# Optimization experiments

Measured on AMD Instinct MI355X. Metric: run time of the kernel, lower is better.

Reference implementation:

```python
import jax, jax.numpy as jnp
import numpy as np

B, N, C = 1, 256, 128        # batch, n_res, norm_channel
H, AC = 4, 32                # num_head, attention_channel


def setup_inputs() -> dict:
    key = jax.random.key(0)
    ks = jax.random.split(key, 9)
    s = 0.02
    return {
        "act": jax.random.normal(ks[0], (B, N, N, C), jnp.float32),
        "mask": jnp.ones((B, N, N), jnp.float32),
        "ln_g": jnp.ones((C,), jnp.float32),
        "ln_b": jnp.zeros((C,), jnp.float32),
        "wq": (jax.random.normal(ks[1], (C, H * AC), jnp.float32) * s),
        "wk": (jax.random.normal(ks[2], (C, H * AC), jnp.float32) * s),
        "wv": (jax.random.normal(ks[3], (C, H * AC), jnp.float32) * s),
        "w2d": (jax.random.normal(ks[4], (C, H), jnp.float32) * s),
        "wg": (jax.random.normal(ks[5], (C, H * AC), jnp.float32) * s),
        "bg": jnp.zeros((H * AC,), jnp.float32),
        "wo": (jax.random.normal(ks[6], (H * AC, C), jnp.float32) * s),
        "bo": jnp.zeros((C,), jnp.float32),
    }


def reference(act, mask, ln_g, ln_b, wq, wk, wv, w2d, wg, bg, wo, bo):
    eps = 1e-5
    mu = jnp.mean(act, axis=-1, keepdims=True)
    var = jnp.mean(jnp.square(act - mu), axis=-1, keepdims=True)
    a = (act - mu) * jax.lax.rsqrt(var + eps) * ln_g + ln_b  # LayerNorm

    b_, m_, i_, _ = a.shape
    q = (a @ wq).reshape(b_, m_, i_, H, AC)
    k = (a @ wk).reshape(b_, m_, i_, H, AC)
    v = (a @ wv).reshape(b_, m_, i_, H, AC)

    factor = 1.0 / np.sqrt(AC).astype(np.float32)
    # mask bias: [b, m, 1, 1, j]
    bias = (1e9 * (mask - 1.0))[:, :, None, None, :]
    aff = jnp.einsum('bmihc,bmjhc->bmhij', q * factor, k) + bias

    # pair bias: [b, h, i, j], broadcast over m (torch trailing-dim broadcast, b=1)
    nb = jnp.einsum('bijc,ch->bhij', a, w2d)
    weights = jax.nn.softmax(aff + nb[:, None], axis=-1)  # [b,m,h,i,j]

    g = jax.nn.sigmoid(a @ wg + bg).reshape(b_, m_, i_, H, AC)
    out = jnp.einsum('bmhqk,bmkhc->bmqhc', weights, v) * g  # [b,m,q,h,c]
    return out.reshape(b_, m_, i_, H * AC) @ wo + bo
```

## Files before the change

kernel.cpp:

```cpp
#include <hip/hip_runtime.h>
#include <hip/hip_fp16.h>
#include <math.h>


#define NRES 256
#define CCH  128
#define NROWS (NRES * NRES)
#define FACTOR 0.17677669529663687f

typedef __attribute__((ext_vector_type(8))) __bf16 bf16x8;
typedef __attribute__((ext_vector_type(4))) float f32x4;

__device__ __forceinline__ f32x4 mfma16(bf16x8 a, bf16x8 b, f32x4 c) {
    return __builtin_amdgcn_mfma_f32_16x16x32_bf16(a, b, c, 0, 0, 0);
}

union PK4 { __bf16 b[4]; uint2 u2; };
union PK2 { __bf16 b[2]; unsigned int u; };

__device__ __forceinline__ void hilo(float x, __bf16& h, __bf16& l) {
    h = (__bf16)x;
    l = (__bf16)(x - (float)h);
}

__global__ __launch_bounds__(256) void prep_kernel(
    const float* __restrict__ wq, const float* __restrict__ wk,
    const float* __restrict__ wv, const float* __restrict__ wg,
    const float* __restrict__ wo,
    __bf16* __restrict__ wph, __bf16* __restrict__ wpl)
{
    const int gid = blockIdx.x * 256 + threadIdx.x;
    const int wid = gid >> 11;
    const int rem = gid & 2047;
    const int nstrip = rem >> 8;
    const int kf = (rem >> 6) & 3;
    const int lane = rem & 63;
    const int l15 = lane & 15, quad = lane >> 4;
    const float* W = (wid == 0) ? wq : (wid == 1) ? wk :
                     (wid == 2) ? wv : (wid == 3) ? wg : wo;
    const float scale = (wid == 0) ? FACTOR : 1.0f;
    bf16x8 hb, lb;
    #pragma unroll
    for (int e = 0; e < 8; ++e) {
        int k = kf * 32 + quad * 8 + e;
        int n = nstrip * 16 + l15;
        float v = W[k * CCH + n] * scale;
        __bf16 h, l; hilo(v, h, l);
        hb[e] = h; lb[e] = l;
    }
    *(bf16x8*)&wph[(size_t)gid * 8] = hb;
    *(bf16x8*)&wpl[(size_t)gid * 8] = lb;
}

__global__ __launch_bounds__(256) void lnproj_kernel(
    const float* __restrict__ act, const float* __restrict__ ln_g,
    const float* __restrict__ ln_b, const float* __restrict__ w2d,
    const __bf16* __restrict__ wph, const float* __restrict__ bg,
    __bf16* __restrict__ qb, __bf16* __restrict__ kb,
    __bf16* __restrict__ vb, __half* __restrict__ gfh,
    float* __restrict__ nbP)
{
    __shared__ __align__(16) char smem[34816];
    const int t = threadIdx.x, w = t >> 6, lane = t & 63;
    const int l15 = lane & 15, quad = lane >> 4;
    __bf16* const aH = (__bf16*)(smem + w * 8704);
    const int r0w = blockIdx.x * 128 + w * 32;

    {
        const int row = lane >> 1, half = lane & 1;
        const int grow = r0w + row;
        const float* __restrict__ xp = act + (size_t)grow * CCH + half * 64;
        float4 x4[16];
        #pragma unroll
        for (int c = 0; c < 16; ++c) x4[c] = *(const float4*)(xp + c * 4);
        float s = 0.f, sq = 0.f;
        #pragma unroll
        for (int c = 0; c < 16; ++c) {
            s  += (x4[c].x + x4[c].y) + (x4[c].z + x4[c].w);
            sq += x4[c].x * x4[c].x + x4[c].y * x4[c].y +
                  x4[c].z * x4[c].z + x4[c].w * x4[c].w;
        }
        s  += __shfl_xor(s, 1, 64);
        sq += __shfl_xor(sq, 1, 64);
        float mu  = s * (1.0f / CCH);
        float var = fmaf(sq, 1.0f / CCH, -mu * mu);
        float rs  = rsqrtf(var + 1e-5f);
        float nb[4] = {0.f, 0.f, 0.f, 0.f};
        const float4* __restrict__ w2d4 = (const float4*)w2d;
        #pragma unroll
        for (int c2 = 0; c2 < 8; ++c2) {
            bf16x8 pk;
            #pragma unroll
            for (int cc = 0; cc < 2; ++cc) {
                const int c = c2 * 2 + cc;
                float4 g4 = *(const float4*)&ln_g[half * 64 + c * 4];
                float4 b4 = *(const float4*)&ln_b[half * 64 + c * 4];
                float* xv = (float*)&x4[c];
                float* gv = (float*)&g4;
                float* bv = (float*)&b4;
                #pragma unroll
                for (int e = 0; e < 4; ++e) {
                    float av = fmaf((xv[e] - mu) * rs, gv[e], bv[e]);
                    pk[cc * 4 + e] = (__bf16)av;
                    float4 wv = w2d4[half * 64 + c * 4 + e];
                    nb[0] = fmaf(av, wv.x, nb[0]);
                    nb[1] = fmaf(av, wv.y, nb[1]);
                    nb[2] = fmaf(av, wv.z, nb[2]);
                    nb[3] = fmaf(av, wv.w, nb[3]);
                }
            }
            *(bf16x8*)&aH[row * 136 + half * 64 + c2 * 8] = pk;
        }
        #pragma unroll
        for (int hh = 0; hh < 4; ++hh)
            nb[hh] += __shfl_xor(nb[hh], 1, 64);
        if (half == 0) {
            const int i = grow >> 8, j = grow & 255;
            #pragma unroll
            for (int hh = 0; hh < 4; ++hh) {
                size_t f = ((size_t)hh << 14) + ((size_t)(i >> 4) << 10) +
                           ((size_t)(j >> 4) << 6) + ((size_t)((j >> 2) & 3) << 4) +
                           (i & 15);
                nbP[f * 4 + (j & 3)] = nb[hh];
            }
        }
    }

    bf16x8 A0[4], A1[4];
    #pragma unroll
    for (int kf = 0; kf < 4; ++kf) {
        const int ao = l15 * 136 + kf * 32 + quad * 8;
        A0[kf] = *(const bf16x8*)&aH[ao];
        A1[kf] = *(const bf16x8*)&aH[ao + 16 * 136];
    }

    #pragma unroll 1
    for (int tn = 0; tn < 4; ++tn) {
        const __bf16* __restrict__ Bh = wph + (size_t)tn * 16384;
        f32x4 acc0[8], acc1[8];
        #pragma unroll
        for (int n = 0; n < 8; ++n) {
            acc0[n] = (f32x4){0.f, 0.f, 0.f, 0.f};
            acc1[n] = (f32x4){0.f, 0.f, 0.f, 0.f};
        }
        #pragma unroll
        for (int kf = 0; kf < 4; ++kf)
            #pragma unroll
            for (int n = 0; n < 8; ++n) {
                bf16x8 bh = *(const bf16x8*)&Bh[(size_t)((n * 4 + kf) * 64 + lane) * 8];
                acc0[n] = mfma16(A0[kf], bh, acc0[n]);
                acc1[n] = mfma16(A1[kf], bh, acc1[n]);
            }

        if (tn == 3) {
            __half* const sth = (__half*)aH;
            #pragma unroll 1
            for (int sp = 0; sp < 2; ++sp) {
                f32x4* accp = sp ? acc1 : acc0;
                #pragma unroll
                for (int n = 0; n < 8; ++n)
                    #pragma unroll
                    for (int r = 0; r < 4; ++r) {
                        float v = accp[n][r] + bg[n * 16 + l15];
                        sth[(quad * 4 + r) * 136 + n * 16 + l15] =
                            (__half)(1.0f / (1.0f + __expf(-v)));
                    }
                #pragma unroll
                for (int i = 0; i < 4; ++i) {
                    int row = i * 4 + (lane >> 4);
                    int c8 = lane & 15;
                    uint4 hv = *(const uint4*)&sth[row * 136 + c8 * 8];
                    *(uint4*)&gfh[(size_t)(r0w + sp * 16 + row) * CCH + c8 * 8] = hv;
                }
            }
        } else {
            __bf16* const sth = (__bf16*)aH;
            __bf16* const oh = (tn == 0) ? qb : (tn == 1) ? kb : vb;
            #pragma unroll 1
            for (int sp = 0; sp < 2; ++sp) {
                f32x4* accp = sp ? acc1 : acc0;
                #pragma unroll
                for (int n = 0; n < 8; ++n)
                    #pragma unroll
                    for (int r = 0; r < 4; ++r)
                        sth[(quad * 4 + r) * 136 + n * 16 + l15] = (__bf16)accp[n][r];
                #pragma unroll
                for (int i = 0; i < 4; ++i) {
                    int row = i * 4 + (lane >> 4);
                    int c8 = lane & 15;
                    uint4 hv = *(const uint4*)&sth[row * 136 + c8 * 8];
                    *(uint4*)&oh[(size_t)(r0w + sp * 16 + row) * CCH + c8 * 8] = hv;
                }
            }
        }
    }
}

__global__ __launch_bounds__(256) void attn_kernel(
    const __bf16* __restrict__ qb, const __bf16* __restrict__ kb,
    const __bf16* __restrict__ vb, const __half* __restrict__ gfh,
    const float* __restrict__ mask, const float* __restrict__ nbP,
    __bf16* __restrict__ gth, __bf16* __restrict__ gtl)
{
    __shared__ __align__(16) char smem[23040];
    __bf16* const vth = (__bf16*)smem;
    __bf16* const pbb = (__bf16*)(smem + 16896);
    float*  const biasrow = (float*)(smem + 22016);
    const int t = threadIdx.x, w = t >> 6, lane = t & 63;
    const int l15 = lane & 15, quad = lane >> 4;
    const int mrow = blockIdx.x >> 2, h = blockIdx.x & 3;
    const size_t rbase = (size_t)mrow * NRES;
    const int ch0 = h * 32;

    biasrow[t] = 1e9f * (mask[mrow * NRES + t] - 1.0f);

    #pragma unroll
    for (int it = 0; it < 4; ++it) {
        int f = t + it * 256;
        int j = f >> 2, cg = f & 3;
        bf16x8 hv = *(const bf16x8*)&vb[(rbase + j) * CCH + ch0 + cg * 8];
        #pragma unroll
        for (int e = 0; e < 8; ++e)
            vth[(cg * 8 + e) * 264 + j] = hv[e];
    }
    __syncthreads();

    const int i0 = w * 64;
    bf16x8 Qh[4];
    #pragma unroll
    for (int s = 0; s < 4; ++s)
        Qh[s] = *(const bf16x8*)&qb[(rbase + i0 + s * 16 + l15) * CCH + ch0 + quad * 8];

    f32x4 O[4][2];
    float ls[4] = {0.f, 0.f, 0.f, 0.f};
    #pragma unroll
    for (int s = 0; s < 4; ++s) {
        O[s][0] = (f32x4){0.f, 0.f, 0.f, 0.f};
        O[s][1] = (f32x4){0.f, 0.f, 0.f, 0.f};
    }
    __bf16* const ph = pbb + w * 640;

    for (int jb = 0; jb < NRES; jb += 32) {
        bf16x8 Kh[2];
        #pragma unroll
        for (int js = 0; js < 2; ++js)
            Kh[js] = *(const bf16x8*)&kb[(rbase + jb + js * 16 + l15) * CCH + ch0 + quad * 8];
        bf16x8 Vh2[2];
        #pragma unroll
        for (int c = 0; c < 2; ++c)
            Vh2[c] = *(const bf16x8*)&vth[(c * 16 + l15) * 264 + jb + quad * 8];
        #pragma unroll
        for (int s = 0; s < 4; ++s) {
            #pragma unroll
            for (int js = 0; js < 2; ++js) {
                f32x4 S = (f32x4){0.f, 0.f, 0.f, 0.f};
                S = mfma16(Kh[js], Qh[s], S);
                size_t f4 = (((size_t)(h * 16 + w * 4 + s) * 16 +
                              (jb >> 4) + js) << 6) + quad * 16 + l15;
                float4 nb4 = *(const float4*)&nbP[f4 * 4];
                float4 mb4 = *(const float4*)&biasrow[jb + js * 16 + quad * 4];
                float p0 = __expf(S[0] + nb4.x + mb4.x - 4.0f);
                float p1 = __expf(S[1] + nb4.y + mb4.y - 4.0f);
                float p2 = __expf(S[2] + nb4.z + mb4.z - 4.0f);
                float p3 = __expf(S[3] + nb4.w + mb4.w - 4.0f);
                ls[s] += (p0 + p1) + (p2 + p3);
                PK4 hh;
                hh.b[0] = (__bf16)p0; hh.b[1] = (__bf16)p1;
                hh.b[2] = (__bf16)p2; hh.b[3] = (__bf16)p3;
                *(uint2*)&ph[l15 * 40 + js * 16 + quad * 4] = hh.u2;
            }
            bf16x8 Ph = *(const bf16x8*)&ph[l15 * 40 + quad * 8];
            #pragma unroll
            for (int c = 0; c < 2; ++c)
                O[s][c] = mfma16(Vh2[c], Ph, O[s][c]);
        }
    }

    #pragma unroll
    for (int s = 0; s < 4; ++s) {
        ls[s] += __shfl_xor(ls[s], 16, 64);
        ls[s] += __shfl_xor(ls[s], 32, 64);
    }

    float ov[4][2][4];
    #pragma unroll
    for (int s = 0; s < 4; ++s) {
        float inv = 1.0f / ls[s];
        #pragma unroll
        for (int c = 0; c < 2; ++c) {
            size_t gi = (rbase + i0 + s * 16 + l15) * CCH + ch0 + c * 16 + quad * 4;
            uint2 gu = *(const uint2*)&gfh[gi];
            const __half* gh = (const __half*)&gu;
            #pragma unroll
            for (int r = 0; r < 4; ++r)
                ov[s][c][r] = O[s][c][r] * inv * (float)gh[r];
        }
    }
    __syncthreads();
    __bf16* const stp = (__bf16*)(smem + w * 5120);
    #pragma unroll
    for (int s = 0; s < 4; ++s)
        #pragma unroll
        for (int c = 0; c < 2; ++c) {
            PK4 hh;
            #pragma unroll
            for (int r = 0; r < 4; ++r) hh.b[r] = (__bf16)ov[s][c][r];
            *(uint2*)&stp[(s * 16 + l15) * 40 + c * 16 + quad * 4] = hh.u2;
        }
    #pragma unroll
    for (int i = 0; i < 4; ++i) {
        int row = i * 16 + (lane >> 2);
        int c8 = lane & 3;
        uint4 hv = *(const uint4*)&stp[row * 40 + c8 * 8];
        *(uint4*)&gth[(rbase + i0 + row) * CCH + ch0 + c8 * 8] = hv;
    }
    #pragma unroll
    for (int s = 0; s < 4; ++s)
        #pragma unroll
        for (int c = 0; c < 2; ++c) {
            PK4 ll;
            #pragma unroll
            for (int r = 0; r < 4; ++r) {
                __bf16 hv = (__bf16)ov[s][c][r];
                ll.b[r] = (__bf16)(ov[s][c][r] - (float)hv);
            }
            *(uint2*)&stp[(s * 16 + l15) * 40 + c * 16 + quad * 4] = ll.u2;
        }
    #pragma unroll
    for (int i = 0; i < 4; ++i) {
        int row = i * 16 + (lane >> 2);
        int c8 = lane & 3;
        uint4 lv = *(const uint4*)&stp[row * 40 + c8 * 8];
        *(uint4*)&gtl[(rbase + i0 + row) * CCH + ch0 + c8 * 8] = lv;
    }
}

__global__ __launch_bounds__(256) void out_kernel(
    const __bf16* __restrict__ gth, const __bf16* __restrict__ gtl,
    const __bf16* __restrict__ wph, const __bf16* __restrict__ wpl,
    const float* __restrict__ bo, float* __restrict__ out)
{
    __shared__ __align__(16) float eps[4][16 * 132];
    const int t = threadIdx.x, w = t >> 6, lane = t & 63;
    const int l15 = lane & 15, quad = lane >> 4;
    const int r0 = blockIdx.x * 64 + w * 16;
    const __bf16* __restrict__ Bh = wph + (size_t)4 * 16384;
    const __bf16* __restrict__ Bl = wpl + (size_t)4 * 16384;

    f32x4 acc[8];
    #pragma unroll
    for (int n = 0; n < 8; ++n) acc[n] = (f32x4){0.f, 0.f, 0.f, 0.f};

    #pragma unroll
    for (int kf = 0; kf < 4; ++kf) {
        size_t idx = (size_t)(r0 + l15) * CCH + kf * 32 + quad * 8;
        bf16x8 Ahf = *(const bf16x8*)&gth[idx];
        bf16x8 Alf = *(const bf16x8*)&gtl[idx];
        #pragma unroll
        for (int n = 0; n < 8; ++n) {
            size_t boff = (size_t)((n * 4 + kf) * 64 + lane) * 8;
            bf16x8 bh = *(const bf16x8*)&Bh[boff];
            bf16x8 bl = *(const bf16x8*)&Bl[boff];
            acc[n] = mfma16(Ahf, bh, acc[n]);
            acc[n] = mfma16(Ahf, bl, acc[n]);
            acc[n] = mfma16(Alf, bh, acc[n]);
        }
    }

    #pragma unroll
    for (int n = 0; n < 8; ++n)
        #pragma unroll
        for (int r = 0; r < 4; ++r)
            eps[w][(quad * 4 + r) * 132 + n * 16 + l15] = acc[n][r];
    const int erow = lane >> 2;
    const int ecg0 = lane & 3;
    #pragma unroll
    for (int it = 0; it < 8; ++it) {
        int cg = ecg0 + it * 4;
        float4 v4 = *(const float4*)&eps[w][erow * 132 + cg * 4];
        float4 b4 = *(const float4*)&bo[cg * 4];
        v4.x += b4.x; v4.y += b4.y; v4.z += b4.z; v4.w += b4.w;
        *(float4*)&out[(size_t)(r0 + erow) * CCH + cg * 4] = v4;
    }
}

extern "C" void kernel_launch(void* const* d_in, const int* in_sizes, int n_in,
                              void* d_out, int out_size, void* d_ws, size_t ws_size,
                              hipStream_t stream)
{
    const float* act  = (const float*)d_in[0];
    const float* mask = (const float*)d_in[1];
    const float* ln_g = (const float*)d_in[2];
    const float* ln_b = (const float*)d_in[3];
    const float* wq   = (const float*)d_in[4];
    const float* wk   = (const float*)d_in[5];
    const float* wv   = (const float*)d_in[6];
    const float* w2d  = (const float*)d_in[7];
    const float* wg   = (const float*)d_in[8];
    const float* bg   = (const float*)d_in[9];
    const float* wo   = (const float*)d_in[10];
    const float* bo   = (const float*)d_in[11];
    float* out = (float*)d_out;

    const size_t SZ = (size_t)NROWS * CCH;
    __bf16* bws = (__bf16*)d_ws;
    __bf16* qb  = bws;
    __bf16* kb  = bws + SZ;
    __bf16* vb  = bws + 2 * SZ;
    __bf16* gth = bws + 3 * SZ;
    __bf16* gtl = bws + 4 * SZ;
    __half* gfh = (__half*)(bws + 5 * SZ);
    float* nbP = (float*)(bws + 6 * SZ);
    __bf16* wph = (__bf16*)(nbP + 4 * NROWS);
    __bf16* wpl = wph + 5 * 16384;

    prep_kernel<<<40, 256, 0, stream>>>(wq, wk, wv, wg, wo, wph, wpl);
    lnproj_kernel<<<512, 256, 0, stream>>>(
        act, ln_g, ln_b, w2d, wph, bg, qb, kb, vb, gfh, nbP);
    attn_kernel<<<NRES * 4, 256, 0, stream>>>(
        qb, kb, vb, gfh, mask, nbP, gth, gtl);
    out_kernel<<<1024, 256, 0, stream>>>(gth, gtl, wph, wpl, bo, out);
}
```

Baseline: 204.7 us.

## Fuse LN-projection, attention and output projection into one per-row mega kernel

Replaces the lnproj, attention and output kernels with a single kernel per m-row (512 threads, ~145KB LDS). Each block does LayerNorm, Q/K/V/gate projections, softmax-attention over all heads, and the output projection. K and transposed V stay in shared memory, and Q and gate stay in registers. The pair bias is computed in a separate small nb_kernel, since it is needed across rows. This removes the global round-trips of q/k/v/gate and gated attention output. In exchange there are only 256 blocks with large LDS, which lowers occupancy, and attention heads are processed sequentially within each block.

```diff
diff --git a/kernel.cpp b/kernel.cpp
--- a/kernel.cpp
+++ b/kernel.cpp
@@ -16,7 +16,6 @@
 }
 
 union PK4 { __bf16 b[4]; uint2 u2; };
-union PK2 { __bf16 b[2]; unsigned int u; };
 
 __device__ __forceinline__ void hilo(float x, __bf16& h, __bf16& l) {
     h = (__bf16)x;
@@ -52,23 +51,105 @@
     *(bf16x8*)&wpl[(size_t)gid * 8] = lb;
 }
 
-__global__ __launch_bounds__(256) void lnproj_kernel(
+__global__ __launch_bounds__(256) void nb_kernel(
     const float* __restrict__ act, const float* __restrict__ ln_g,
     const float* __restrict__ ln_b, const float* __restrict__ w2d,
-    const __bf16* __restrict__ wph, const float* __restrict__ bg,
-    __bf16* __restrict__ qb, __bf16* __restrict__ kb,
-    __bf16* __restrict__ vb, __half* __restrict__ gfh,
     float* __restrict__ nbP)
 {
-    __shared__ __align__(16) char smem[34816];
+    const int t = threadIdx.x, w = t >> 6, lane = t & 63;
+    const int r0w = blockIdx.x * 128 + w * 32;
+    const int row = lane >> 1, half = lane & 1;
+    const int grow = r0w + row;
+    const float* __restrict__ xp = act + (size_t)grow * CCH + half * 64;
+    float4 x4[16];
+    #pragma unroll
+    for (int c = 0; c < 16; ++c) x4[c] = *(const float4*)(xp + c * 4);
+    float s = 0.f, sq = 0.f;
+    #pragma unroll
+    for (int c = 0; c < 16; ++c) {
+        s  += (x4[c].x + x4[c].y) + (x4[c].z + x4[c].w);
+        sq += x4[c].x * x4[c].x + x4[c].y * x4[c].y +
+              x4[c].z * x4[c].z + x4[c].w * x4[c].w;
+    }
+    s  += __shfl_xor(s, 1, 64);
+    sq += __shfl_xor(sq, 1, 64);
+    float mu  = s * (1.0f / CCH);
+    float var = fmaf(sq, 1.0f / CCH, -mu * mu);
+    float rs  = rsqrtf(var + 1e-5f);
+    float nb[4] = {0.f, 0.f, 0.f, 0.f};
+    const float4* __restrict__ w2d4 = (const float4*)w2d;
+    #pragma unroll
+    for (int c = 0; c < 16; ++c) {
+        float4 g4 = *(const float4*)&ln_g[half * 64 + c * 4];
+        float4 b4 = *(const float4*)&ln_b[half * 64 + c * 4];
+        float* xv = (float*)&x4[c];
+        float* gv = (float*)&g4;
+        float* bv = (float*)&b4;
+        #pragma unroll
+        for (int e = 0; e < 4; ++e) {
+            float av = fmaf((xv[e] - mu) * rs, gv[e], bv[e]);
+            float4 wv = w2d4[half * 64 + c * 4 + e];
+            nb[0] = fmaf(av, wv.x, nb[0]);
+            nb[1] = fmaf(av, wv.y, nb[1]);
+            nb[2] = fmaf(av, wv.z, nb[2]);
+            nb[3] = fmaf(av, wv.w, nb[3]);
+        }
+    }
+    #pragma unroll
+    for (int hh = 0; hh < 4; ++hh)
+        nb[hh] += __shfl_xor(nb[hh], 1, 64);
+    if (half == 0) {
+        const int i = grow >> 8, j = grow & 255;
+        #pragma unroll
+        for (int hh = 0; hh < 4; ++hh) {
+            size_t f = ((size_t)hh << 14) + ((size_t)(i >> 4) << 10) +
+                       ((size_t)(j >> 4) << 6) + ((size_t)((j >> 2) & 3) << 4) +
+                       (i & 15);
+            nbP[f * 4 + (j & 3)] = nb[hh];
+        }
+    }
+}
+
+__device__ __forceinline__ void proj32(const bf16x8* A0, const bf16x8* A1,
+    const __bf16* __restrict__ Bh, int lane, f32x4* acc0, f32x4* acc1)
+{
+    #pragma unroll
+    for (int n = 0; n < 8; ++n) {
+        acc0[n] = (f32x4){0.f, 0.f, 0.f, 0.f};
+        acc1[n] = (f32x4){0.f, 0.f, 0.f, 0.f};
+    }
+    #pragma unroll
+    for (int kf = 0; kf < 4; ++kf)
+        #pragma unroll
+        for (int n = 0; n < 8; ++n) {
+            bf16x8 bh = *(const bf16x8*)&Bh[(size_t)((n * 4 + kf) * 64 + lane) * 8];
+            acc0[n] = mfma16(A0[kf], bh, acc0[n]);
+            acc1[n] = mfma16(A1[kf], bh, acc1[n]);
+        }
+}
+
+__global__ __launch_bounds__(512) void mega_kernel(
+    const float* __restrict__ act, const float* __restrict__ ln_g,
+    const float* __restrict__ ln_b, const __bf16* __restrict__ wph,
+    const __bf16* __restrict__ wpl, const float* __restrict__ bg,
+    const float* __restrict__ mask, const float* __restrict__ nbP,
+    const float* __restrict__ bo, float* __restrict__ out)
+{
+    __shared__ __align__(16) char smem[148480];
     const int t = threadIdx.x, w = t >> 6, lane = t & 63;
     const int l15 = lane & 15, quad = lane >> 4;
+    const int m = blockIdx.x;
+    __bf16* const Kl = (__bf16*)smem;
     __bf16* const aH = (__bf16*)(smem + w * 8704);
-    const int r0w = blockIdx.x * 128 + w * 32;
+    __bf16* const VT = (__bf16*)(smem + 69632);
+    __bf16* const ph = (__bf16*)(smem + 137216 + w * 1280);
+    float*  const biasrow = (float*)(smem + 147456);
+
+    if (t < 256) biasrow[t] = 1e9f * (mask[m * NRES + t] - 1.0f);
 
     {
         const int row = lane >> 1, half = lane & 1;
-        const int grow = r0w + row;
+        const int grow = m * NRES + w * 32 + row;
         const float* __restrict__ xp = act + (size_t)grow * CCH + half * 64;
         float4 x4[16];
         #pragma unroll
@@ -85,8 +166,6 @@
         float mu  = s * (1.0f / CCH);
         float var = fmaf(sq, 1.0f / CCH, -mu * mu);
         float rs  = rsqrtf(var + 1e-5f);
-        float nb[4] = {0.f, 0.f, 0.f, 0.f};
-        const float4* __restrict__ w2d4 = (const float4*)w2d;
         #pragma unroll
         for (int c2 = 0; c2 < 8; ++c2) {
             bf16x8 pk;
@@ -99,30 +178,10 @@
                 float* gv = (float*)&g4;
                 float* bv = (float*)&b4;
                 #pragma unroll
-                for (int e = 0; e < 4; ++e) {
-                    float av = fmaf((xv[e] - mu) * rs, gv[e], bv[e]);
-                    pk[cc * 4 + e] = (__bf16)av;
-                    float4 wv = w2d4[half * 64 + c * 4 + e];
-                    nb[0] = fmaf(av, wv.x, nb[0]);
-                    nb[1] = fmaf(av, wv.y, nb[1]);
-                    nb[2] = fmaf(av, wv.z, nb[2]);
-                    nb[3] = fmaf(av, wv.w, nb[3]);
-                }
+                for (int e = 0; e < 4; ++e)
+                    pk[cc * 4 + e] = (__bf16)fmaf((xv[e] - mu) * rs, gv[e], bv[e]);
             }
             *(bf16x8*)&aH[row * 136 + half * 64 + c2 * 8] = pk;
-        }
-        #pragma unroll
-        for (int hh = 0; hh < 4; ++hh)
-            nb[hh] += __shfl_xor(nb[hh], 1, 64);
-        if (half == 0) {
-            const int i = grow >> 8, j = grow & 255;
-            #pragma unroll
-            for (int hh = 0; hh < 4; ++hh) {
-                size_t f = ((size_t)hh << 14) + ((size_t)(i >> 4) << 10) +
-                           ((size_t)(j >> 4) << 6) + ((size_t)((j >> 2) & 3) << 4) +
-                           (i & 15);
-                nbP[f * 4 + (j & 3)] = nb[hh];
-            }
         }
     }
 
@@ -134,10 +193,187 @@
         A1[kf] = *(const bf16x8*)&aH[ao + 16 * 136];
     }
 
-    #pragma unroll 1
-    for (int tn = 0; tn < 4; ++tn) {
-        const __bf16* __restrict__ Bh = wph + (size_t)tn * 16384;
-        f32x4 acc0[8], acc1[8];
+    f32x4 acc0[8], acc1[8];
+    bf16x8 Qh[4][2];
+    uint2  greg[4][2][2];
+
+    proj32(A0, A1, wph, lane, acc0, acc1);
+    {
+        __bf16* const sth = aH;
+        #pragma unroll
+        for (int sp = 0; sp < 2; ++sp) {
+            f32x4* accp = sp ? acc1 : acc0;
+            #pragma unroll
+            for (int n = 0; n < 8; ++n)
+                #pragma unroll
+                for (int r = 0; r < 4; ++r)
+                    sth[(quad * 4 + r) * 136 + n * 16 + l15] = (__bf16)accp[n][r];
+            #pragma unroll
+            for (int h = 0; h < 4; ++h)
+                Qh[h][sp] = *(const bf16x8*)&sth[l15 * 136 + h * 32 + quad * 8];
+        }
+    }
+
+    proj32(A0, A1, wph + 3 * 16384, lane, acc0, acc1);
+    {
+        __half* const sthH = (__half*)aH;
+        #pragma unroll
+        for (int sp = 0; sp < 2; ++sp) {
+            f32x4* accp = sp ? acc1 : acc0;
+            #pragma unroll
+            for (int n = 0; n < 8; ++n)
+                #pragma unroll
+                for (int r = 0; r < 4; ++r) {
+                    float v = accp[n][r] + bg[n * 16 + l15];
+                    sthH[(quad * 4 + r) * 136 + n * 16 + l15] =
+                        (__half)(1.0f / (1.0f + __expf(-v)));
+                }
+            #pragma unroll
+            for (int h = 0; h < 4; ++h)
+                #pragma unroll
+                for (int c = 0; c < 2; ++c)
+                    greg[h][sp][c] =
+                        *(const uint2*)&sthH[l15 * 136 + h * 32 + c * 16 + quad * 4];
+        }
+    }
+
+    proj32(A0, A1, wph + 1 * 16384, lane, acc0, acc1);
+    {
+        __bf16* const Kp = aH;
+        #pragma unroll
+        for (int sp = 0; sp < 2; ++sp) {
+            f32x4* accp = sp ? acc1 : acc0;
+            #pragma unroll
+            for (int n = 0; n < 8; ++n)
+                #pragma unroll
+                for (int r = 0; r < 4; ++r)
+                    Kp[(sp * 16 + quad * 4 + r) * 136 + n * 16 + l15] =
+                        (__bf16)accp[n][r];
+        }
+    }
+
+    proj32(A0, A1, wph + 2 * 16384, lane, acc0, acc1);
+    {
+        const int jbase = w * 32;
+        #pragma unroll
+        for (int sp = 0; sp < 2; ++sp) {
+            f32x4* accp = sp ? acc1 : acc0;
+            #pragma unroll
+            for (int n = 0; n < 8; ++n)
+                #pragma unroll
+                for (int r = 0; r < 4; ++r)
+                    VT[(n * 16 + l15) * 264 + jbase + sp * 16 + quad * 4 + r] =
+                        (__bf16)accp[n][r];
+        }
+    }
+    __syncthreads();
+
+    uint2 ovh[4][2][2], ovl[4][2][2];
+    #pragma unroll
+    for (int h = 0; h < 4; ++h) {
+        f32x4 O[2][2];
+        float ls[2] = {0.f, 0.f};
+        #pragma unroll
+        for (int s = 0; s < 2; ++s) {
+            O[s][0] = (f32x4){0.f, 0.f, 0.f, 0.f};
+            O[s][1] = (f32x4){0.f, 0.f, 0.f, 0.f};
+        }
+        #pragma unroll 1
+        for (int jb = 0; jb < NRES; jb += 32) {
+            bf16x8 Kh[2];
+            #pragma unroll
+            for (int js = 0; js < 2; ++js)
+                Kh[js] = *(const bf16x8*)&Kl[(jb + js * 16 + l15) * 136 +
+                                             h * 32 + quad * 8];
+            bf16x8 Vh2[2];
+            #pragma unroll
+            for (int c = 0; c < 2; ++c)
+                Vh2[c] = *(const bf16x8*)&VT[(h * 32 + c * 16 + l15) * 264 +
+                                             jb + quad * 8];
+            #pragma unroll
+            for (int s = 0; s < 2; ++s) {
+                #pragma unroll
+                for (int js = 0; js < 2; ++js) {
+                    f32x4 S = (f32x4){0.f, 0.f, 0.f, 0.f};
+                    S = mfma16(Kh[js], Qh[h][s], S);
+                    size_t f4 = (size_t)h * 16384 + (size_t)(w * 2 + s) * 1024 +
+                                (size_t)((jb >> 4) + js) * 64 + quad * 16 + l15;
+                    float4 nb4 = *(const float4*)&nbP[f4 * 4];
+                    float4 mb4 = *(const float4*)&biasrow[jb + js * 16 + quad * 4];
+                    float p0 = __expf(S[0] + nb4.x + mb4.x - 4.0f);
+                    float p1 = __expf(S[1] + nb4.y + mb4.y - 4.0f);
+                    float p2 = __expf(S[2] + nb4.z + mb4.z - 4.0f);
+                    float p3 = __expf(S[3] + nb4.w + mb4.w - 4.0f);
+                    ls[s] += (p0 + p1) + (p2 + p3);
+                    PK4 hh;
+                    hh.b[0] = (__bf16)p0; hh.b[1] = (__bf16)p1;
+                    hh.b[2] = (__bf16)p2; hh.b[3] = (__bf16)p3;
+                    *(uint2*)&ph[l15 * 40 + js * 16 + quad * 4] = hh.u2;
+                }
+                bf16x8 Ph = *(const bf16x8*)&ph[l15 * 40 + quad * 8];
+                #pragma unroll
+                for (int c = 0; c < 2; ++c)
+                    O[s][c] = mfma16(Vh2[c], Ph, O[s][c]);
+            }
+        }
+        #pragma unroll
+        for (int s = 0; s < 2; ++s) {
+            ls[s] += __shfl_xor(ls[s], 16, 64);
+            ls[s] += __shfl_xor(ls[s], 32, 64);
+        }
+        #pragma unroll
+        for (int s = 0; s < 2; ++s) {
+            float inv = 1.0f / ls[s];
+            #pragma unroll
+            for (int c = 0; c < 2; ++c) {
+                const __half* gh = (const __half*)&greg[h][s][c];
+                PK4 hh, lo;
+                #pragma unroll
+                for (int r = 0; r < 4; ++r) {
+                    float v = O[s][c][r] * inv * (float)gh[r];
+                    __bf16 hb; __bf16 lb; hilo(v, hb, lb);
+                    hh.b[r] = hb; lo.b[r] = lb;
+                }
+                ovh[h][s][c] = hh.u2;
+                ovl[h][s][c] = lo.u2;
+            }
+        }
+    }
+    __syncthreads();
+
+    {
+        __bf16* const sth = aH;
+        #pragma unroll
+        for (int h = 0; h < 4; ++h)
+            #pragma unroll
+            for (int s = 0; s < 2; ++s)
+                #pragma unroll
+                for (int c = 0; c < 2; ++c)
+                    *(uint2*)&sth[(s * 16 + l15) * 136 + h * 32 + c * 16 + quad * 4] =
+                        ovh[h][s][c];
+        bf16x8 Ah0[4], Ah1[4];
+        #pragma unroll
+        for (int kf = 0; kf < 4; ++kf) {
+            Ah0[kf] = *(const bf16x8*)&sth[l15 * 136 + kf * 32 + quad * 8];
+            Ah1[kf] = *(const bf16x8*)&sth[(16 + l15) * 136 + kf * 32 + quad * 8];
+        }
+        #pragma unroll
+        for (int h = 0; h < 4; ++h)
+            #pragma unroll
+            for (int s = 0; s < 2; ++s)
+                #pragma unroll
+                for (int c = 0; c < 2; ++c)
+                    *(uint2*)&sth[(s * 16 + l15) * 136 + h * 32 + c * 16 + quad * 4] =
+                        ovl[h][s][c];
+        bf16x8 Al0[4], Al1[4];
+        #pragma unroll
+        for (int kf = 0; kf < 4; ++kf) {
+            Al0[kf] = *(const bf16x8*)&sth[l15 * 136 + kf * 32 + quad * 8];
+            Al1[kf] = *(const bf16x8*)&sth[(16 + l15) * 136 + kf * 32 + quad * 8];
+        }
+
+        const __bf16* __restrict__ Bh = wph + (size_t)4 * 16384;
+        const __bf16* __restrict__ Bl = wpl + (size_t)4 * 16384;
         #pragma unroll
         for (int n = 0; n < 8; ++n) {
             acc0[n] = (f32x4){0.f, 0.f, 0.f, 0.f};
@@ -147,240 +383,27 @@
         for (int kf = 0; kf < 4; ++kf)
             #pragma unroll
             for (int n = 0; n < 8; ++n) {
-                bf16x8 bh = *(const bf16x8*)&Bh[(size_t)((n * 4 + kf) * 64 + lane) * 8];
-                acc0[n] = mfma16(A0[kf], bh, acc0[n]);
-                acc1[n] = mfma16(A1[kf], bh, acc1[n]);
+                size_t boff = (size_t)((n * 4 + kf) * 64 + lane) * 8;
+                bf16x8 bh = *(const bf16x8*)&Bh[boff];
+                bf16x8 bl = *(const bf16x8*)&Bl[boff];
+                acc0[n] = mfma16(Ah0[kf], bh, acc0[n]);
+                acc0[n] = mfma16(Ah0[kf], bl, acc0[n]);
+                acc0[n] = mfma16(Al0[kf], bh, acc0[n]);
+                acc1[n] = mfma16(Ah1[kf], bh, acc1[n]);
+                acc1[n] = mfma16(Ah1[kf], bl, acc1[n]);
+                acc1[n] = mfma16(Al1[kf], bh, acc1[n]);
             }
 
-        if (tn == 3) {
-            __half* const sth = (__half*)aH;
-            #pragma unroll 1
-            for (int sp = 0; sp < 2; ++sp) {
-                f32x4* accp = sp ? acc1 : acc0;
-                #pragma unroll
-                for (int n = 0; n < 8; ++n)
-                    #pragma unroll
-                    for (int r = 0; r < 4; ++r) {
-                        float v = accp[n][r] + bg[n * 16 + l15];
-                        sth[(quad * 4 + r) * 136 + n * 16 + l15] =
-                            (__half)(1.0f / (1.0f + __expf(-v)));
-                    }
-                #pragma unroll
-                for (int i = 0; i < 4; ++i) {
-                    int row = i * 4 + (lane >> 4);
-                    int c8 = lane & 15;
-                    uint4 hv = *(const uint4*)&sth[row * 136 + c8 * 8];
-                    *(uint4*)&gfh[(size_t)(r0w + sp * 16 + row) * CCH + c8 * 8] = hv;
-                }
+        const size_t rbase = (size_t)m * NRES + w * 32;
+        #pragma unroll
+        for (int n = 0; n < 8; ++n) {
+            float b = bo[n * 16 + l15];
+            #pragma unroll
+            for (int r = 0; r < 4; ++r) {
+                out[(rbase + quad * 4 + r) * CCH + n * 16 + l15] = acc0[n][r] + b;
+                out[(rbase + 16 + quad * 4 + r) * CCH + n * 16 + l15] = acc1[n][r] + b;
             }
-        } else {
-            __bf16* const sth = (__bf16*)aH;
-            __bf16* const oh = (tn == 0) ? qb : (tn == 1) ? kb : vb;
-            #pragma unroll 1
-            for (int sp = 0; sp < 2; ++sp) {
-                f32x4* accp = sp ? acc1 : acc0;
-                #pragma unroll
-                for (int n = 0; n < 8; ++n)
-                    #pragma unroll
-                    for (int r = 0; r < 4; ++r)
-                        sth[(quad * 4 + r) * 136 + n * 16 + l15] = (__bf16)accp[n][r];
-                #pragma unroll
-                for (int i = 0; i < 4; ++i) {
-                    int row = i * 4 + (lane >> 4);
-                    int c8 = lane & 15;
-                    uint4 hv = *(const uint4*)&sth[row * 136 + c8 * 8];
-                    *(uint4*)&oh[(size_t)(r0w + sp * 16 + row) * CCH + c8 * 8] = hv;
-                }
-            }
-        }
-    }
-}
-
-__global__ __launch_bounds__(256) void attn_kernel(
-    const __bf16* __restrict__ qb, const __bf16* __restrict__ kb,
-    const __bf16* __restrict__ vb, const __half* __restrict__ gfh,
-    const float* __restrict__ mask, const float* __restrict__ nbP,
-    __bf16* __restrict__ gth, __bf16* __restrict__ gtl)
-{
-    __shared__ __align__(16) char smem[23040];
-    __bf16* const vth = (__bf16*)smem;
-    __bf16* const pbb = (__bf16*)(smem + 16896);
-    float*  const biasrow = (float*)(smem + 22016);
-    const int t = threadIdx.x, w = t >> 6, lane = t & 63;
-    const int l15 = lane & 15, quad = lane >> 4;
-    const int mrow = blockIdx.x >> 2, h = blockIdx.x & 3;
-    const size_t rbase = (size_t)mrow * NRES;
-    const int ch0 = h * 32;
-
-    biasrow[t] = 1e9f * (mask[mrow * NRES + t] - 1.0f);
-
-    #pragma unroll
-    for (int it = 0; it < 4; ++it) {
-        int f = t + it * 256;
-        int j = f >> 2, cg = f & 3;
-        bf16x8 hv = *(const bf16x8*)&vb[(rbase + j) * CCH + ch0 + cg * 8];
-        #pragma unroll
-        for (int e = 0; e < 8; ++e)
-            vth[(cg * 8 + e) * 264 + j] = hv[e];
-    }
-    __syncthreads();
-
-    const int i0 = w * 64;
-    bf16x8 Qh[4];
-    #pragma unroll
-    for (int s = 0; s < 4; ++s)
-        Qh[s] = *(const bf16x8*)&qb[(rbase + i0 + s * 16 + l15) * CCH + ch0 + quad * 8];
-
-    f32x4 O[4][2];
-    float ls[4] = {0.f, 0.f, 0.f, 0.f};
-    #pragma unroll
-    for (int s = 0; s < 4; ++s) {
-        O[s][0] = (f32x4){0.f, 0.f, 0.f, 0.f};
-        O[s][1] = (f32x4){0.f, 0.f, 0.f, 0.f};
-    }
-    __bf16* const ph = pbb + w * 640;
-
-    for (int jb = 0; jb < NRES; jb += 32) {
-        bf16x8 Kh[2];
-        #pragma unroll
-        for (int js = 0; js < 2; ++js)
-            Kh[js] = *(const bf16x8*)&kb[(rbase + jb + js * 16 + l15) * CCH + ch0 + quad * 8];
-        bf16x8 Vh2[2];
-        #pragma unroll
-        for (int c = 0; c < 2; ++c)
-            Vh2[c] = *(const bf16x8*)&vth[(c * 16 + l15) * 264 + jb + quad * 8];
-        #pragma unroll
-        for (int s = 0; s < 4; ++s) {
-            #pragma unroll
-            for (int js = 0; js < 2; ++js) {
-                f32x4 S = (f32x4){0.f, 0.f, 0.f, 0.f};
-                S = mfma16(Kh[js], Qh[s], S);
-                size_t f4 = (((size_t)(h * 16 + w * 4 + s) * 16 +
-                              (jb >> 4) + js) << 6) + quad * 16 + l15;
-                float4 nb4 = *(const float4*)&nbP[f4 * 4];
-                float4 mb4 = *(const float4*)&biasrow[jb + js * 16 + quad * 4];
-                float p0 = __expf(S[0] + nb4.x + mb4.x - 4.0f);
-                float p1 = __expf(S[1] + nb4.y + mb4.y - 4.0f);
-                float p2 = __expf(S[2] + nb4.z + mb4.z - 4.0f);
-                float p3 = __expf(S[3] + nb4.w + mb4.w - 4.0f);
-                ls[s] += (p0 + p1) + (p2 + p3);
-                PK4 hh;
-                hh.b[0] = (__bf16)p0; hh.b[1] = (__bf16)p1;
-                hh.b[2] = (__bf16)p2; hh.b[3] = (__bf16)p3;
-                *(uint2*)&ph[l15 * 40 + js * 16 + quad * 4] = hh.u2;
-            }
-            bf16x8 Ph = *(const bf16x8*)&ph[l15 * 40 + quad * 8];
-            #pragma unroll
-            for (int c = 0; c < 2; ++c)
-                O[s][c] = mfma16(Vh2[c], Ph, O[s][c]);
-        }
-    }
-
-    #pragma unroll
-    for (int s = 0; s < 4; ++s) {
-        ls[s] += __shfl_xor(ls[s], 16, 64);
-        ls[s] += __shfl_xor(ls[s], 32, 64);
-    }
-
-    float ov[4][2][4];
-    #pragma unroll
-    for (int s = 0; s < 4; ++s) {
-        float inv = 1.0f / ls[s];
-        #pragma unroll
-        for (int c = 0; c < 2; ++c) {
-            size_t gi = (rbase + i0 + s * 16 + l15) * CCH + ch0 + c * 16 + quad * 4;
-            uint2 gu = *(const uint2*)&gfh[gi];
-            const __half* gh = (const __half*)&gu;
-            #pragma unroll
-            for (int r = 0; r < 4; ++r)
-                ov[s][c][r] = O[s][c][r] * inv * (float)gh[r];
-        }
-    }
-    __syncthreads();
-    __bf16* const stp = (__bf16*)(smem + w * 5120);
-    #pragma unroll
-    for (int s = 0; s < 4; ++s)
-        #pragma unroll
-        for (int c = 0; c < 2; ++c) {
-            PK4 hh;
-            #pragma unroll
-            for (int r = 0; r < 4; ++r) hh.b[r] = (__bf16)ov[s][c][r];
-            *(uint2*)&stp[(s * 16 + l15) * 40 + c * 16 + quad * 4] = hh.u2;
-        }
-    #pragma unroll
-    for (int i = 0; i < 4; ++i) {
-        int row = i * 16 + (lane >> 2);
-        int c8 = lane & 3;
-        uint4 hv = *(const uint4*)&stp[row * 40 + c8 * 8];
-        *(uint4*)&gth[(rbase + i0 + row) * CCH + ch0 + c8 * 8] = hv;
-    }
-    #pragma unroll
-    for (int s = 0; s < 4; ++s)
-        #pragma unroll
-        for (int c = 0; c < 2; ++c) {
-            PK4 ll;
-            #pragma unroll
-            for (int r = 0; r < 4; ++r) {
-                __bf16 hv = (__bf16)ov[s][c][r];
-                ll.b[r] = (__bf16)(ov[s][c][r] - (float)hv);
-            }
-            *(uint2*)&stp[(s * 16 + l15) * 40 + c * 16 + quad * 4] = ll.u2;
-        }
-    #pragma unroll
-    for (int i = 0; i < 4; ++i) {
-        int row = i * 16 + (lane >> 2);
-        int c8 = lane & 3;
-        uint4 lv = *(const uint4*)&stp[row * 40 + c8 * 8];
-        *(uint4*)&gtl[(rbase + i0 + row) * CCH + ch0 + c8 * 8] = lv;
-    }
-}
-
-__global__ __launch_bounds__(256) void out_kernel(
-    const __bf16* __restrict__ gth, const __bf16* __restrict__ gtl,
-    const __bf16* __restrict__ wph, const __bf16* __restrict__ wpl,
-    const float* __restrict__ bo, float* __restrict__ out)
-{
-    __shared__ __align__(16) float eps[4][16 * 132];
-    const int t = threadIdx.x, w = t >> 6, lane = t & 63;
-    const int l15 = lane & 15, quad = lane >> 4;
-    const int r0 = blockIdx.x * 64 + w * 16;
-    const __bf16* __restrict__ Bh = wph + (size_t)4 * 16384;
-    const __bf16* __restrict__ Bl = wpl + (size_t)4 * 16384;
-
-    f32x4 acc[8];
-    #pragma unroll
-    for (int n = 0; n < 8; ++n) acc[n] = (f32x4){0.f, 0.f, 0.f, 0.f};
-
-    #pragma unroll
-    for (int kf = 0; kf < 4; ++kf) {
-        size_t idx = (size_t)(r0 + l15) * CCH + kf * 32 + quad * 8;
-        bf16x8 Ahf = *(const bf16x8*)&gth[idx];
-        bf16x8 Alf = *(const bf16x8*)&gtl[idx];
-        #pragma unroll
-        for (int n = 0; n < 8; ++n) {
-            size_t boff = (size_t)((n * 4 + kf) * 64 + lane) * 8;
-            bf16x8 bh = *(const bf16x8*)&Bh[boff];
-            bf16x8 bl = *(const bf16x8*)&Bl[boff];
-            acc[n] = mfma16(Ahf, bh, acc[n]);
-            acc[n] = mfma16(Ahf, bl, acc[n]);
-            acc[n] = mfma16(Alf, bh, acc[n]);
-        }
-    }
-
-    #pragma unroll
-    for (int n = 0; n < 8; ++n)
-        #pragma unroll
-        for (int r = 0; r < 4; ++r)
-            eps[w][(quad * 4 + r) * 132 + n * 16 + l15] = acc[n][r];
-    const int erow = lane >> 2;
-    const int ecg0 = lane & 3;
-    #pragma unroll
-    for (int it = 0; it < 8; ++it) {
-        int cg = ecg0 + it * 4;
-        float4 v4 = *(const float4*)&eps[w][erow * 132 + cg * 4];
-        float4 b4 = *(const float4*)&bo[cg * 4];
-        v4.x += b4.x; v4.y += b4.y; v4.z += b4.z; v4.w += b4.w;
-        *(float4*)&out[(size_t)(r0 + erow) * CCH + cg * 4] = v4;
+        }
     }
 }
 
@@ -402,22 +425,12 @@
     const float* bo   = (const float*)d_in[11];
     float* out = (float*)d_out;
 
-    const size_t SZ = (size_t)NROWS * CCH;
-    __bf16* bws = (__bf16*)d_ws;
-    __bf16* qb  = bws;
-    __bf16* kb  = bws + SZ;
-    __bf16* vb  = bws + 2 * SZ;
-    __bf16* gth = bws + 3 * SZ;
-    __bf16* gtl = bws + 4 * SZ;
-    __half* gfh = (__half*)(bws + 5 * SZ);
-    float* nbP = (float*)(bws + 6 * SZ);
+    float* nbP = (float*)d_ws;
     __bf16* wph = (__bf16*)(nbP + 4 * NROWS);
     __bf16* wpl = wph + 5 * 16384;
 
     prep_kernel<<<40, 256, 0, stream>>>(wq, wk, wv, wg, wo, wph, wpl);
-    lnproj_kernel<<<512, 256, 0, stream>>>(
-        act, ln_g, ln_b, w2d, wph, bg, qb, kb, vb, gfh, nbP);
-    attn_kernel<<<NRES * 4, 256, 0, stream>>>(
-        qb, kb, vb, gfh, mask, nbP, gth, gtl);
-    out_kernel<<<1024, 256, 0, stream>>>(gth, gtl, wph, wpl, bo, out);
-}
+    nb_kernel<<<512, 256, 0, stream>>>(act, ln_g, ln_b, w2d, nbP);
+    mega_kernel<<<256, 512, 0, stream>>>(
+        act, ln_g, ln_b, wph, wpl, bg, mask, nbP, bo, out);
+}
```

New measurement: 193.8 us. 1.06x faster.
